# Optimization experiments

Hardware: AMD Instinct MI355X
Metric: run time of the kernel (lower is better)

The kernel has to match this reference:

```python
import jax, jax.numpy as jnp
import numpy as np

N = 30000        # nodes
E = 480000       # edges
IN = 256         # input feature dim
D = 32           # num_hidden per head
H = 4            # heads for layers 0,1
C = 47           # num_classes (final layer, 1 head)
NEG_SLOPE = 0.2


def setup_inputs() -> dict:
    key = jax.random.key(0)
    ks = jax.random.split(key, 16)
    def glorot(k, shape):
        fan = sum(shape)
        return jax.random.normal(k, shape, jnp.float32) * jnp.sqrt(2.0 / fan)
    inp = {
        "x": jax.random.normal(ks[0], (N, IN), jnp.float32),
        # layer 0: IN -> H*D, no residual
        "W0": glorot(ks[1], (IN, H * D)),
        "al0": glorot(ks[2], (H, D)),
        "ar0": glorot(ks[3], (H, D)),
        # layer 1: H*D -> H*D, residual fc
        "W1": glorot(ks[4], (H * D, H * D)),
        "resW1": glorot(ks[5], (H * D, H * D)),
        "al1": glorot(ks[6], (H, D)),
        "ar1": glorot(ks[7], (H, D)),
        # final layer: H*D -> 1*C, residual fc
        "W2": glorot(ks[8], (H * D, 1 * C)),
        "resW2": glorot(ks[9], (H * D, 1 * C)),
        "al2": glorot(ks[10], (1, C)),
        "ar2": glorot(ks[11], (1, C)),
        "src": jax.random.randint(ks[12], (E,), 0, N, jnp.int32),
        "dst": jax.random.randint(ks[13], (E,), 0, N, jnp.int32),
    }
    return inp


def gat_layer(h, W, al, ar, src, dst, heads, d, resW=None, act=None):
    # h: [N, F_in]; W: [F_in, heads*d]; al/ar: [heads, d]
    n = h.shape[0]
    feat = (h @ W).reshape(n, heads, d)                 # [N, H, D]
    el = (feat * al).sum(-1)                            # [N, H]
    er = (feat * ar).sum(-1)                            # [N, H]
    e = jax.nn.leaky_relu(el[src] + er[dst], NEG_SLOPE)  # [E, H]
    # edge softmax over incoming edges of each dst node (numerically stable)
    emax = jax.ops.segment_max(e, dst, num_segments=n)  # [N, H]
    emax = jnp.where(jnp.isfinite(emax), emax, 0.0)     # guard empty segments
    w = jnp.exp(e - emax[dst])                          # [E, H]
    wsum = jax.ops.segment_sum(w, dst, num_segments=n)  # [N, H]
    a = w / jnp.maximum(wsum[dst], 1e-9)                # [E, H]
    msg = feat[src] * a[:, :, None]                     # [E, H, D]
    rst = jax.ops.segment_sum(msg, dst, num_segments=n)  # [N, H, D]
    if resW is not None:
        rst = rst + (h @ resW).reshape(n, heads, d)
    if act is not None:
        rst = act(rst)
    return rst, e


def reference(x, W0, al0, ar0, W1, resW1, al1, ar1, W2, resW2, al2, ar2, src, dst):
    act = jax.nn.elu
    # layer 0 (no residual, no in-conv activation), then flatten + activation
    h, e0 = gat_layer(x, W0, al0, ar0, src, dst, H, D)
    h = act(h.reshape(N, H * D))
    # layer 1 (residual, in-conv activation), then flatten + activation
    h, e1 = gat_layer(h, W1, al1, ar1, src, dst, H, D, resW=resW1, act=act)
    h = act(h.reshape(N, H * D))
    # final layer (residual, no activation), mean over heads
    h, e2 = gat_layer(h, W2, al2, ar2, src, dst, 1, C, resW=resW2)
    logits = h.mean(axis=1)                             # [N, C]
    return (logits, e0, e1, e2)
```

## Files before the change

kernel.cpp:

```cpp
#include <hip/hip_runtime.h>
#include <hip/hip_bf16.h>
#include <math.h>

#define NN 30000
#define NE 480000
#define FIN 256
#define DH 32
#define NH 4
#define NC 47
#define NODE_BLKS 7500
#define EDGE_BLKS 1875
#define SCAN_CHUNK 1024
#define NCHUNKS 30

typedef __attribute__((ext_vector_type(8))) short frag_ab;
typedef __attribute__((ext_vector_type(4))) float f32x4;
typedef __hip_bfloat16 bf16;

static inline size_t align256(size_t x) { return (x + 255) & ~(size_t)255; }

__device__ __forceinline__ short f2bf(float f) {
    union { float f; unsigned u; } c; c.f = f;
    unsigned r = (c.u + 0x7FFFu + ((c.u >> 16) & 1u)) >> 16;
    return (short)r;
}
__device__ __forceinline__ float b2f(unsigned short u) {
    union { unsigned u; float f; } c; c.u = (unsigned)u << 16; return c.f;
}
__device__ __forceinline__ float expw(float v) {
    return __expf((v >= 0.f) ? v : 0.2f * v);
}
__device__ __forceinline__ float lrelu(float v) {
    return (v >= 0.f) ? v : 0.2f * v;
}

__global__ void prep_count(const float* __restrict__ W0, const float* __restrict__ W1,
                           const float* __restrict__ rW1, const float* __restrict__ W2,
                           const float* __restrict__ rW2,
                           const float* __restrict__ al0, const float* __restrict__ ar0,
                           const float* __restrict__ al1, const float* __restrict__ ar1,
                           const float* __restrict__ al2, const float* __restrict__ ar2,
                           bf16* __restrict__ W0t, bf16* __restrict__ W1t,
                           bf16* __restrict__ rW1t, bf16* __restrict__ W2t,
                           bf16* __restrict__ rW2t,
                           const int* __restrict__ dst, int* __restrict__ cnt,
                           int* __restrict__ rank) {
    if (blockIdx.y == 5) {
        int e = blockIdx.x * 256 + threadIdx.x;
        if (e < NE) rank[e] = atomicAdd(&cnt[dst[e]], 1);
        return;
    }
    const float *W, *al, *ar; bf16* Wt; int K, Msrc, Mpad, rows, H, D;
    switch (blockIdx.y) {
        case 0: W = W0;  Wt = W0t;  K = 256; Msrc = 128; Mpad = 128; rows = 144; H = 4; D = 32; al = al0; ar = ar0; break;
        case 1: W = W1;  Wt = W1t;  K = 128; Msrc = 128; Mpad = 128; rows = 144; H = 4; D = 32; al = al1; ar = ar1; break;
        case 2: W = rW1; Wt = rW1t; K = 128; Msrc = 128; Mpad = 128; rows = 128; H = 0; D = 0;  al = nullptr; ar = nullptr; break;
        case 3: W = W2;  Wt = W2t;  K = 128; Msrc = 47;  Mpad = 48;  rows = 64;  H = 1; D = 47; al = al2; ar = ar2; break;
        default: W = rW2; Wt = rW2t; K = 128; Msrc = 47; Mpad = 48;  rows = 48;  H = 0; D = 0;  al = nullptr; ar = nullptr; break;
    }
    int i = blockIdx.x * 256 + threadIdx.x;
    if (i >= rows * K) return;
    int row = i / K, k = i - row * K;
    float v = 0.f;
    if (row < Msrc) {
        v = W[(long)k * Msrc + row];
    } else if (H > 0 && row >= Mpad && row < Mpad + 2 * H) {
        int idx = row - Mpad;
        int h = (idx < H) ? idx : idx - H;
        const float* a = (idx < H) ? al : ar;
        float s = 0.f;
        for (int d = 0; d < D; ++d) s += W[(long)k * Msrc + h * D + d] * a[h * D + d];
        v = s;
    }
    Wt[i] = __float2bfloat16(v);
}

__global__ void fill_k(const int* __restrict__ dst, const int* __restrict__ src,
                       const int* __restrict__ rank, const int* __restrict__ loff,
                       const int* __restrict__ bases, int* __restrict__ srcs) {
    int e = blockIdx.x * blockDim.x + threadIdx.x;
    if (e < NE) {
        const int d = dst[e];
        srcs[loff[d] + bases[d >> 10] + rank[e]] = src[e];
    }
}

template <bool A_F32, int NT1, int NT2, int HH, int TAIL>
__global__ __launch_bounds__(256) void gemm_mfma(
    const void* __restrict__ Av, const bf16* __restrict__ B1t,
    const bf16* __restrict__ B2t,
    bf16* __restrict__ C1b, float* __restrict__ el, float* __restrict__ er,
    bf16* __restrict__ C2, int N, int K, int M, int nGemmBlocks,
    const int* __restrict__ t_cnt, int* __restrict__ t_loff, int* __restrict__ t_bsum,
    int* __restrict__ t_bases, int* __restrict__ t_done,
    const float4* __restrict__ pel, const float4* __restrict__ per,
    const int* __restrict__ src, const int* __restrict__ dst,
    float* __restrict__ eout) {
    constexpr int LP = 56;
    __shared__ bf16 As[64][LP];
    __shared__ bf16 Bs1[NT1 * 16][LP];
    __shared__ bf16 Bs2[(NT2 > 0) ? NT2 * 16 : 1][LP];
    __shared__ int ws4[4];

    const int tid = threadIdx.x;

    if constexpr (TAIL == 1) {
        if (blockIdx.x >= nGemmBlocks) {
            const int chunk = blockIdx.x - nGemmBlocks;
            const int lane = tid & 63;
            const int wid = tid >> 6;
            const int g = chunk * SCAN_CHUNK + tid * 4;
            const int a0 = (g + 0 < NN) ? t_cnt[g + 0] : 0;
            const int a1 = (g + 1 < NN) ? t_cnt[g + 1] : 0;
            const int a2 = (g + 2 < NN) ? t_cnt[g + 2] : 0;
            const int a3 = (g + 3 < NN) ? t_cnt[g + 3] : 0;
            const int lsum = a0 + a1 + a2 + a3;
            int x = lsum;
            #pragma unroll
            for (int off = 1; off < 64; off <<= 1) {
                int y = __shfl_up(x, off);
                if (lane >= off) x += y;
            }
            if (lane == 63) ws4[wid] = x;
            __syncthreads();
            int wbase = 0;
            #pragma unroll
            for (int j = 0; j < 4; ++j) if (j < wid) wbase += ws4[j];
            const int excl = wbase + x - lsum;
            if (g + 0 < NN) t_loff[g + 0] = excl;
            if (g + 1 < NN) t_loff[g + 1] = excl + a0;
            if (g + 2 < NN) t_loff[g + 2] = excl + a0 + a1;
            if (g + 3 < NN) t_loff[g + 3] = excl + a0 + a1 + a2;
            if (tid == 0) {
                t_bsum[chunk] = ws4[0] + ws4[1] + ws4[2] + ws4[3];
                __threadfence();
                const int prev = atomicAdd(t_done, 1);
                if (prev == NCHUNKS - 1) {
                    __threadfence();
                    int acc = 0;
                    for (int j = 0; j < NCHUNKS; ++j) { t_bases[j] = acc; acc += t_bsum[j]; }
                    t_bases[NCHUNKS] = acc;
                }
            }
            return;
        }
    }
    if constexpr (TAIL == 2) {
        if (blockIdx.x >= nGemmBlocks) {
            const int e = (blockIdx.x - nGemmBlocks) * 256 + tid;
            const int s = src[e], d = dst[e];
            const float4 a = pel[s], b = per[d];
            float4 v;
            v.x = lrelu(a.x + b.x); v.y = lrelu(a.y + b.y);
            v.z = lrelu(a.z + b.z); v.w = lrelu(a.w + b.w);
            *reinterpret_cast<float4*>(eout + e * 4) = v;
            return;
        }
    }

    const int lane = tid & 63;
    const int wid = tid >> 6;
    const int row0 = blockIdx.x * 64;
    const int l15 = lane & 15;
    const int kq = lane >> 4;

    f32x4 acc1[NT1], acc2[(NT2 > 0) ? NT2 : 1];
    #pragma unroll
    for (int t = 0; t < NT1; ++t) acc1[t] = (f32x4){0.f, 0.f, 0.f, 0.f};
    if constexpr (NT2 > 0) {
        #pragma unroll
        for (int t = 0; t < NT2; ++t) acc2[t] = (f32x4){0.f, 0.f, 0.f, 0.f};
    }

    for (int k0 = 0; k0 < K; k0 += 32) {
        {
            const int r = tid >> 2, kk = (tid & 3) * 8;
            const int gr = row0 + r;
            if constexpr (A_F32) {
                const float* A = (const float*)Av;
                short tmp[8];
                if (gr < N) {
                    const float4 v0 = *(const float4*)&A[(long)gr * K + k0 + kk];
                    const float4 v1 = *(const float4*)&A[(long)gr * K + k0 + kk + 4];
                    tmp[0] = f2bf(v0.x); tmp[1] = f2bf(v0.y); tmp[2] = f2bf(v0.z); tmp[3] = f2bf(v0.w);
                    tmp[4] = f2bf(v1.x); tmp[5] = f2bf(v1.y); tmp[6] = f2bf(v1.z); tmp[7] = f2bf(v1.w);
                } else {
                    #pragma unroll
                    for (int j = 0; j < 8; ++j) tmp[j] = 0;
                }
                *(frag_ab*)&As[r][kk] = *(const frag_ab*)tmp;
            } else {
                const bf16* A = (const bf16*)Av;
                frag_ab v = {0, 0, 0, 0, 0, 0, 0, 0};
                if (gr < N) v = *(const frag_ab*)&A[(long)gr * K + k0 + kk];
                *(frag_ab*)&As[r][kk] = v;
            }
        }
        for (int i = tid; i < NT1 * 64; i += 256) {
            const int c = i >> 2, kk = (i & 3) * 8;
            *(frag_ab*)&Bs1[c][kk] = *(const frag_ab*)&B1t[(long)c * K + k0 + kk];
        }
        if constexpr (NT2 > 0) {
            for (int i = tid; i < NT2 * 64; i += 256) {
                const int c = i >> 2, kk = (i & 3) * 8;
                *(frag_ab*)&Bs2[c][kk] = *(const frag_ab*)&B2t[(long)c * K + k0 + kk];
            }
        }
        __syncthreads();

        const frag_ab a = *(const frag_ab*)&As[wid * 16 + l15][kq * 8];
        #pragma unroll
        for (int t = 0; t < NT1; ++t) {
            const frag_ab b = *(const frag_ab*)&Bs1[t * 16 + l15][kq * 8];
            acc1[t] = __builtin_amdgcn_mfma_f32_16x16x32_bf16(a, b, acc1[t], 0, 0, 0);
        }
        if constexpr (NT2 > 0) {
            #pragma unroll
            for (int t = 0; t < NT2; ++t) {
                const frag_ab b = *(const frag_ab*)&Bs2[t * 16 + l15][kq * 8];
                acc2[t] = __builtin_amdgcn_mfma_f32_16x16x32_bf16(a, b, acc2[t], 0, 0, 0);
            }
        }
        __syncthreads();
    }

    const int r0 = row0 + wid * 16 + kq * 4;
    #pragma unroll
    for (int t = 0; t < NT1; ++t) {
        const int c = t * 16 + l15;
        #pragma unroll
        for (int reg = 0; reg < 4; ++reg) {
            const int r = r0 + reg;
            if (r >= N) continue;
            const float v = acc1[t][reg];
            if (c < M) {
                C1b[(long)r * M + c] = __float2bfloat16(v);
            } else if (c < M + HH) {
                el[(long)r * HH + (c - M)] = v;
            } else if (c < M + 2 * HH) {
                er[(long)r * HH + (c - M - HH)] = v;
            }
        }
    }
    if constexpr (NT2 > 0) {
        #pragma unroll
        for (int t = 0; t < NT2; ++t) {
            const int c = t * 16 + l15;
            if (c >= M) continue;
            #pragma unroll
            for (int reg = 0; reg < 4; ++reg) {
                const int r = r0 + reg;
                if (r < N) C2[(long)r * M + c] = __float2bfloat16(acc2[t][reg]);
            }
        }
    }
}

template <int NELU, bool HAS_RES>
__global__ __launch_bounds__(256) void node_agg4(
    const bf16* __restrict__ featb, const float* __restrict__ el,
    const float4* __restrict__ er4,
    const int* __restrict__ loff, const int* __restrict__ bases,
    const int* __restrict__ srcs,
    const bf16* __restrict__ res, bf16* __restrict__ out) {
    const int node = (int)((blockIdx.x * blockDim.x + threadIdx.x) >> 6);
    const int lane = threadIdx.x & 63;
    const int beg = loff[node] + bases[node >> 10];
    const int end = (node == NN - 1) ? NE : loff[node + 1] + bases[(node + 1) >> 10];

    const int q = lane >> 4;
    const int l15 = lane & 15;
    const int fi = l15 * 8;
    const int h = l15 >> 2;
    const float4 ern4 = er4[node];
    const float ern = (h == 0) ? ern4.x : (h == 1) ? ern4.y : (h == 2) ? ern4.z : ern4.w;

    float a[8] = {0.f, 0.f, 0.f, 0.f, 0.f, 0.f, 0.f, 0.f};
    float sl = 0.f;
    int i = beg + q;
    for (; i + 4 < end; i += 8) {
        const int iB = i + 4;
        const int snA = srcs[i], snB = srcs[iB];
        const float wA = expw(el[snA * 4 + h] + ern);
        const float wB = expw(el[snB * 4 + h] + ern);
        sl += wA + wB;
        const frag_ab fA = *(const frag_ab*)(featb + (long)snA * 128 + fi);
        const frag_ab fB = *(const frag_ab*)(featb + (long)snB * 128 + fi);
        #pragma unroll
        for (int j = 0; j < 8; ++j)
            a[j] += wA * b2f((unsigned short)fA[j]) + wB * b2f((unsigned short)fB[j]);
    }
    for (; i < end; i += 4) {
        const int sn = srcs[i];
        const float w = expw(el[sn * 4 + h] + ern);
        sl += w;
        const frag_ab f = *(const frag_ab*)(featb + (long)sn * 128 + fi);
        #pragma unroll
        for (int j = 0; j < 8; ++j) a[j] += w * b2f((unsigned short)f[j]);
    }
    sl += __shfl_xor(sl, 16);
    sl += __shfl_xor(sl, 32);
    #pragma unroll
    for (int j = 0; j < 8; ++j) {
        a[j] += __shfl_xor(a[j], 16);
        a[j] += __shfl_xor(a[j], 32);
    }

    if (lane < 16) {
        const float inv = 1.f / fmaxf(sl, 1e-9f);
        float v[8];
        #pragma unroll
        for (int j = 0; j < 8; ++j) v[j] = a[j] * inv;
        if constexpr (HAS_RES) {
            const frag_ab rr = *(const frag_ab*)(res + (long)node * 128 + fi);
            #pragma unroll
            for (int j = 0; j < 8; ++j) v[j] += b2f((unsigned short)rr[j]);
        }
        #pragma unroll
        for (int t = 0; t < NELU; ++t)
            #pragma unroll
            for (int j = 0; j < 8; ++j)
                v[j] = (v[j] > 0.f) ? v[j] : expm1f(v[j]);
        frag_ab o;
        #pragma unroll
        for (int j = 0; j < 8; ++j) o[j] = f2bf(v[j]);
        *(frag_ab*)(out + (long)node * 128 + fi) = o;
    }
}

__global__ __launch_bounds__(256) void final_k(
    const bf16* __restrict__ featb48, const float* __restrict__ el2s,
    const float* __restrict__ er2s,
    const int* __restrict__ loff, const int* __restrict__ bases,
    const int* __restrict__ srcs,
    const bf16* __restrict__ res48, float* __restrict__ logits,
    const int* __restrict__ src, const int* __restrict__ dst,
    float* __restrict__ e2) {
    if (blockIdx.x < NODE_BLKS) {
        const int node = (int)((blockIdx.x * blockDim.x + threadIdx.x) >> 6);
        const int lane = threadIdx.x & 63;
        const int beg = loff[node] + bases[node >> 10];
        const int end = (node == NN - 1) ? NE : loff[node + 1] + bases[(node + 1) >> 10];
        const float ern = er2s[node];

        const int half = lane >> 5;
        const int l31 = lane & 31;
        const bool act = l31 < 24;
        const int fi = l31 * 2;

        float a0 = 0.f, a1 = 0.f, sl = 0.f;
        int i = beg + half;
        for (; i + 2 < end; i += 4) {
            const int iB = i + 2;
            const int snA = srcs[i], snB = srcs[iB];
            const float wA = expw(el2s[snA] + ern);
            const float wB = expw(el2s[snB] + ern);
            sl += wA + wB;
            if (act) {
                const ushort2 fA = *(const ushort2*)(featb48 + (long)snA * 48 + fi);
                const ushort2 fB = *(const ushort2*)(featb48 + (long)snB * 48 + fi);
                a0 += wA * b2f(fA.x) + wB * b2f(fB.x);
                a1 += wA * b2f(fA.y) + wB * b2f(fB.y);
            }
        }
        for (; i < end; i += 2) {
            const int sn = srcs[i];
            const float w = expw(el2s[sn] + ern);
            sl += w;
            if (act) {
                const ushort2 f = *(const ushort2*)(featb48 + (long)sn * 48 + fi);
                a0 += w * b2f(f.x);
                a1 += w * b2f(f.y);
            }
        }
        const float s = __shfl(sl, 0) + __shfl(sl, 32);
        a0 += __shfl_xor(a0, 32);
        a1 += __shfl_xor(a1, 32);

        if (lane < 24) {
            const float inv = 1.f / fmaxf(s, 1e-9f);
            const ushort2 rr = *(const ushort2*)(res48 + (long)node * 48 + fi);
            const float v0 = a0 * inv + b2f(rr.x);
            const float v1 = a1 * inv + b2f(rr.y);
            logits[(long)node * NC + fi] = v0;
            if (fi + 1 < NC) logits[(long)node * NC + fi + 1] = v1;
        }
    } else {
        const int e = (blockIdx.x - NODE_BLKS) * 256 + threadIdx.x;
        e2[e] = lrelu(el2s[src[e]] + er2s[dst[e]]);
    }
}

extern "C" void kernel_launch(void* const* d_in, const int* in_sizes, int n_in,
                              void* d_out, int out_size, void* d_ws, size_t ws_size,
                              hipStream_t stream) {
    const float* x     = (const float*)d_in[0];
    const float* W0    = (const float*)d_in[1];
    const float* al0   = (const float*)d_in[2];
    const float* ar0   = (const float*)d_in[3];
    const float* W1    = (const float*)d_in[4];
    const float* resW1 = (const float*)d_in[5];
    const float* al1   = (const float*)d_in[6];
    const float* ar1   = (const float*)d_in[7];
    const float* W2    = (const float*)d_in[8];
    const float* resW2 = (const float*)d_in[9];
    const float* al2   = (const float*)d_in[10];
    const float* ar2   = (const float*)d_in[11];
    const int*   src   = (const int*)d_in[12];
    const int*   dst   = (const int*)d_in[13];

    float* out    = (float*)d_out;
    float* logits = out;
    float* e0     = out + (long)NN * NC;
    float* e1     = e0 + (long)NE * NH;
    float* e2     = e1 + (long)NE * NH;

    char* p = (char*)d_ws;
    int* cnt    = (int*)p; p += align256(sizeof(int) * (NN + 64));
    int* done   = cnt + NN;
    int* loff   = (int*)p; p += align256(sizeof(int) * (NN + 1));
    int* bsum   = (int*)p; p += align256(sizeof(int) * 32);
    int* bases  = (int*)p; p += align256(sizeof(int) * 32);
    int* rank   = (int*)p; p += align256(sizeof(int) * NE);
    int* srcs   = (int*)p; p += align256(sizeof(int) * NE);
    float* el0b = (float*)p; p += align256(sizeof(float) * NN * NH);
    float* er0b = (float*)p; p += align256(sizeof(float) * NN * NH);
    float* el1b = (float*)p; p += align256(sizeof(float) * NN * NH);
    float* er1b = (float*)p; p += align256(sizeof(float) * NN * NH);
    float* el2b = (float*)p; p += align256(sizeof(float) * NN);
    float* er2b = (float*)p; p += align256(sizeof(float) * NN);
    bf16* resb  = (bf16*)p; p += align256(sizeof(bf16) * (long)NN * 128);
    bf16* featb = (bf16*)p; p += align256(sizeof(bf16) * (long)NN * 128);
    bf16* hb    = (bf16*)p; p += align256(sizeof(bf16) * (long)NN * 128);
    bf16* W0t   = (bf16*)p; p += align256(sizeof(bf16) * 144 * 256);
    bf16* W1t   = (bf16*)p; p += align256(sizeof(bf16) * 144 * 128);
    bf16* rW1t  = (bf16*)p; p += align256(sizeof(bf16) * 128 * 128);
    bf16* W2t   = (bf16*)p; p += align256(sizeof(bf16) * 64 * 128);
    bf16* rW2t  = (bf16*)p; p += align256(sizeof(bf16) * 48 * 128);

    const int gemmBlocks = (NN + 63) / 64;

    hipMemsetAsync(cnt, 0, sizeof(int) * (NN + 64), stream);
    prep_count<<<dim3(EDGE_BLKS, 6), 256, 0, stream>>>(
        W0, W1, resW1, W2, resW2, al0, ar0, al1, ar1, al2, ar2,
        W0t, W1t, rW1t, W2t, rW2t, dst, cnt, rank);

    gemm_mfma<true, 9, 0, NH, 1><<<gemmBlocks + NCHUNKS, 256, 0, stream>>>(
        x, W0t, nullptr, featb, el0b, er0b, nullptr, NN, FIN, 128, gemmBlocks,
        cnt, loff, bsum, bases, done, nullptr, nullptr, nullptr, nullptr, nullptr);

    fill_k<<<EDGE_BLKS, 256, 0, stream>>>(dst, src, rank, loff, bases, srcs);

    node_agg4<1, false><<<NODE_BLKS, 256, 0, stream>>>(
        featb, el0b, (const float4*)er0b, loff, bases, srcs, nullptr, hb);

    gemm_mfma<false, 9, 8, NH, 2><<<gemmBlocks + EDGE_BLKS, 256, 0, stream>>>(
        hb, W1t, rW1t, featb, el1b, er1b, resb, NN, 128, 128, gemmBlocks,
        nullptr, nullptr, nullptr, nullptr, nullptr,
        (const float4*)el0b, (const float4*)er0b, src, dst, e0);

    node_agg4<2, true><<<NODE_BLKS, 256, 0, stream>>>(
        featb, el1b, (const float4*)er1b, loff, bases, srcs, resb, hb);

    gemm_mfma<false, 4, 3, 1, 2><<<gemmBlocks + EDGE_BLKS, 256, 0, stream>>>(
        hb, W2t, rW2t, featb, el2b, er2b, resb, NN, 128, 48, gemmBlocks,
        nullptr, nullptr, nullptr, nullptr, nullptr,
        (const float4*)el1b, (const float4*)er1b, src, dst, e1);

    final_k<<<NODE_BLKS + EDGE_BLKS, 256, 0, stream>>>(
        featb, el2b, er2b, loff, bases, srcs, resb, logits, src, dst, e2);
}
```

Baseline: 176.1 us.

## Fuse CSR fill into first GEMM launch via spin-wait flag; unroll aggregation loops

```diff
diff --git a/kernel.cpp b/kernel.cpp
--- a/kernel.cpp
+++ b/kernel.cpp
@@ -75,16 +75,6 @@
     Wt[i] = __float2bfloat16(v);
 }
 
-__global__ void fill_k(const int* __restrict__ dst, const int* __restrict__ src,
-                       const int* __restrict__ rank, const int* __restrict__ loff,
-                       const int* __restrict__ bases, int* __restrict__ srcs) {
-    int e = blockIdx.x * blockDim.x + threadIdx.x;
-    if (e < NE) {
-        const int d = dst[e];
-        srcs[loff[d] + bases[d >> 10] + rank[e]] = src[e];
-    }
-}
-
 template <bool A_F32, int NT1, int NT2, int HH, int TAIL>
 __global__ __launch_bounds__(256) void gemm_mfma(
     const void* __restrict__ Av, const bf16* __restrict__ B1t,
@@ -92,7 +82,8 @@
     bf16* __restrict__ C1b, float* __restrict__ el, float* __restrict__ er,
     bf16* __restrict__ C2, int N, int K, int M, int nGemmBlocks,
     const int* __restrict__ t_cnt, int* __restrict__ t_loff, int* __restrict__ t_bsum,
-    int* __restrict__ t_bases, int* __restrict__ t_done,
+    int* __restrict__ t_bases, int* __restrict__ t_done, int* __restrict__ t_ready,
+    const int* __restrict__ rank, int* __restrict__ srcs,
     const float4* __restrict__ pel, const float4* __restrict__ per,
     const int* __restrict__ src, const int* __restrict__ dst,
     float* __restrict__ eout) {
@@ -105,6 +96,17 @@
     const int tid = threadIdx.x;
 
     if constexpr (TAIL == 1) {
+        if (blockIdx.x >= nGemmBlocks + NCHUNKS) {
+            if (tid == 0) {
+                while (__hip_atomic_load(t_ready, __ATOMIC_ACQUIRE,
+                                         __HIP_MEMORY_SCOPE_AGENT) == 0) {}
+            }
+            __syncthreads();
+            const int e = (blockIdx.x - nGemmBlocks - NCHUNKS) * 256 + tid;
+            const int d = dst[e];
+            srcs[t_loff[d] + t_bases[d >> 10] + rank[e]] = src[e];
+            return;
+        }
         if (blockIdx.x >= nGemmBlocks) {
             const int chunk = blockIdx.x - nGemmBlocks;
             const int lane = tid & 63;
@@ -131,6 +133,7 @@
             if (g + 1 < NN) t_loff[g + 1] = excl + a0;
             if (g + 2 < NN) t_loff[g + 2] = excl + a0 + a1;
             if (g + 3 < NN) t_loff[g + 3] = excl + a0 + a1 + a2;
+            __syncthreads();
             if (tid == 0) {
                 t_bsum[chunk] = ws4[0] + ws4[1] + ws4[2] + ws4[3];
                 __threadfence();
@@ -140,6 +143,9 @@
                     int acc = 0;
                     for (int j = 0; j < NCHUNKS; ++j) { t_bases[j] = acc; acc += t_bsum[j]; }
                     t_bases[NCHUNKS] = acc;
+                    __threadfence();
+                    __hip_atomic_store(t_ready, 1, __ATOMIC_RELEASE,
+                                       __HIP_MEMORY_SCOPE_AGENT);
                 }
             }
             return;
@@ -278,17 +284,32 @@
     float a[8] = {0.f, 0.f, 0.f, 0.f, 0.f, 0.f, 0.f, 0.f};
     float sl = 0.f;
     int i = beg + q;
+    for (; i + 12 < end; i += 16) {
+        const int s0 = srcs[i], s1 = srcs[i + 4], s2 = srcs[i + 8], s3 = srcs[i + 12];
+        const float w0 = expw(el[s0 * 4 + h] + ern);
+        const float w1 = expw(el[s1 * 4 + h] + ern);
+        const float w2 = expw(el[s2 * 4 + h] + ern);
+        const float w3 = expw(el[s3 * 4 + h] + ern);
+        sl += (w0 + w1) + (w2 + w3);
+        const frag_ab f0 = *(const frag_ab*)(featb + (long)s0 * 128 + fi);
+        const frag_ab f1 = *(const frag_ab*)(featb + (long)s1 * 128 + fi);
+        const frag_ab f2 = *(const frag_ab*)(featb + (long)s2 * 128 + fi);
+        const frag_ab f3 = *(const frag_ab*)(featb + (long)s3 * 128 + fi);
+        #pragma unroll
+        for (int j = 0; j < 8; ++j)
+            a[j] += (w0 * b2f((unsigned short)f0[j]) + w1 * b2f((unsigned short)f1[j]))
+                  + (w2 * b2f((unsigned short)f2[j]) + w3 * b2f((unsigned short)f3[j]));
+    }
     for (; i + 4 < end; i += 8) {
-        const int iB = i + 4;
-        const int snA = srcs[i], snB = srcs[iB];
-        const float wA = expw(el[snA * 4 + h] + ern);
-        const float wB = expw(el[snB * 4 + h] + ern);
-        sl += wA + wB;
-        const frag_ab fA = *(const frag_ab*)(featb + (long)snA * 128 + fi);
-        const frag_ab fB = *(const frag_ab*)(featb + (long)snB * 128 + fi);
+        const int s0 = srcs[i], s1 = srcs[i + 4];
+        const float w0 = expw(el[s0 * 4 + h] + ern);
+        const float w1 = expw(el[s1 * 4 + h] + ern);
+        sl += w0 + w1;
+        const frag_ab f0 = *(const frag_ab*)(featb + (long)s0 * 128 + fi);
+        const frag_ab f1 = *(const frag_ab*)(featb + (long)s1 * 128 + fi);
         #pragma unroll
         for (int j = 0; j < 8; ++j)
-            a[j] += wA * b2f((unsigned short)fA[j]) + wB * b2f((unsigned short)fB[j]);
+            a[j] += w0 * b2f((unsigned short)f0[j]) + w1 * b2f((unsigned short)f1[j]);
     }
     for (; i < end; i += 4) {
         const int sn = srcs[i];
@@ -350,17 +371,20 @@
 
         float a0 = 0.f, a1 = 0.f, sl = 0.f;
         int i = beg + half;
-        for (; i + 2 < end; i += 4) {
-            const int iB = i + 2;
-            const int snA = srcs[i], snB = srcs[iB];
-            const float wA = expw(el2s[snA] + ern);
-            const float wB = expw(el2s[snB] + ern);
-            sl += wA + wB;
+        for (; i + 6 < end; i += 8) {
+            const int s0 = srcs[i], s1 = srcs[i + 2], s2 = srcs[i + 4], s3 = srcs[i + 6];
+            const float w0 = expw(el2s[s0] + ern);
+            const float w1 = expw(el2s[s1] + ern);
+            const float w2 = expw(el2s[s2] + ern);
+            const float w3 = expw(el2s[s3] + ern);
+            sl += (w0 + w1) + (w2 + w3);
             if (act) {
-                const ushort2 fA = *(const ushort2*)(featb48 + (long)snA * 48 + fi);
-                const ushort2 fB = *(const ushort2*)(featb48 + (long)snB * 48 + fi);
-                a0 += wA * b2f(fA.x) + wB * b2f(fB.x);
-                a1 += wA * b2f(fA.y) + wB * b2f(fB.y);
+                const ushort2 f0 = *(const ushort2*)(featb48 + (long)s0 * 48 + fi);
+                const ushort2 f1 = *(const ushort2*)(featb48 + (long)s1 * 48 + fi);
+                const ushort2 f2 = *(const ushort2*)(featb48 + (long)s2 * 48 + fi);
+                const ushort2 f3 = *(const ushort2*)(featb48 + (long)s3 * 48 + fi);
+                a0 += (w0 * b2f(f0.x) + w1 * b2f(f1.x)) + (w2 * b2f(f2.x) + w3 * b2f(f3.x));
+                a1 += (w0 * b2f(f0.y) + w1 * b2f(f1.y)) + (w2 * b2f(f2.y) + w3 * b2f(f3.y));
             }
         }
         for (; i < end; i += 2) {
@@ -418,6 +442,7 @@
     char* p = (char*)d_ws;
     int* cnt    = (int*)p; p += align256(sizeof(int) * (NN + 64));
     int* done   = cnt + NN;
+    int* ready  = cnt + NN + 1;
     int* loff   = (int*)p; p += align256(sizeof(int) * (NN + 1));
     int* bsum   = (int*)p; p += align256(sizeof(int) * 32);
     int* bases  = (int*)p; p += align256(sizeof(int) * 32);
@@ -445,18 +470,17 @@
         W0, W1, resW1, W2, resW2, al0, ar0, al1, ar1, al2, ar2,
         W0t, W1t, rW1t, W2t, rW2t, dst, cnt, rank);
 
-    gemm_mfma<true, 9, 0, NH, 1><<<gemmBlocks + NCHUNKS, 256, 0, stream>>>(
+    gemm_mfma<true, 9, 0, NH, 1><<<gemmBlocks + NCHUNKS + EDGE_BLKS, 256, 0, stream>>>(
         x, W0t, nullptr, featb, el0b, er0b, nullptr, NN, FIN, 128, gemmBlocks,
-        cnt, loff, bsum, bases, done, nullptr, nullptr, nullptr, nullptr, nullptr);
-
-    fill_k<<<EDGE_BLKS, 256, 0, stream>>>(dst, src, rank, loff, bases, srcs);
+        cnt, loff, bsum, bases, done, ready, rank, srcs,
+        nullptr, nullptr, src, dst, nullptr);
 
     node_agg4<1, false><<<NODE_BLKS, 256, 0, stream>>>(
         featb, el0b, (const float4*)er0b, loff, bases, srcs, nullptr, hb);
 
     gemm_mfma<false, 9, 8, NH, 2><<<gemmBlocks + EDGE_BLKS, 256, 0, stream>>>(
         hb, W1t, rW1t, featb, el1b, er1b, resb, NN, 128, 128, gemmBlocks,
-        nullptr, nullptr, nullptr, nullptr, nullptr,
+        nullptr, nullptr, nullptr, nullptr, nullptr, nullptr, nullptr, nullptr,
         (const float4*)el0b, (const float4*)er0b, src, dst, e0);
 
     node_agg4<2, true><<<NODE_BLKS, 256, 0, stream>>>(
@@ -464,7 +488,7 @@
 
     gemm_mfma<false, 4, 3, 1, 2><<<gemmBlocks + EDGE_BLKS, 256, 0, stream>>>(
         hb, W2t, rW2t, featb, el2b, er2b, resb, NN, 128, 48, gemmBlocks,
-        nullptr, nullptr, nullptr, nullptr, nullptr,
+        nullptr, nullptr, nullptr, nullptr, nullptr, nullptr, nullptr, nullptr,
         (const float4*)el1b, (const float4*)er1b, src, dst, e1);
 
     final_k<<<NODE_BLKS + EDGE_BLKS, 256, 0, stream>>>(
```

Result: slower. 232.3 us (+31.9%).
